# Kernel tuning notes

Measured on AMD Instinct MI355X. Metric: run time of the kernel, lower is better.

Reference implementation:

```python
import jax, jax.numpy as jnp
import numpy as np

WINDOW = 128
CAUSAL = True
LOOK_BACKWARD = 1
LOOK_FORWARD = 0  # causal forces look_forward = 0


def _look_around(x, backward, forward, pad_value, dim):
    # pad along window axis (axis=1), then concat shifted slices along `dim`
    nw = x.shape[1]
    pad_cfg = [(0, 0)] * x.ndim
    pad_cfg[1] = (backward, forward)
    padded = jnp.pad(x, pad_cfg, constant_values=pad_value)
    slices = [padded[:, i:i + nw] for i in range(forward + backward + 1)]
    return jnp.concatenate(slices, axis=dim)


def setup_inputs() -> dict:
    key = jax.random.key(0)
    kq, kk, kv = jax.random.split(key, 3)
    shape = (2, 16, 4096, 64)
    return {
        "q": jax.random.normal(kq, shape, dtype=jnp.float32),
        "k": jax.random.normal(kk, shape, dtype=jnp.float32),
        "v": jax.random.normal(kv, shape, dtype=jnp.float32),
    }


def reference(q, k, v):
    b, h, t, e = q.shape
    scale = e ** (-0.5)
    windows = t // WINDOW  # t assumed divisible by WINDOW (pad_to_multiple is no-op)

    # merge batch and heads, bucket into windows
    bq = q.reshape(b * h, windows, WINDOW, e)
    bk = k.reshape(b * h, windows, WINDOW, e)
    bv = v.reshape(b * h, windows, WINDOW, e)

    # look-around gather of key/value windows: j-dim = WINDOW*(1+back+fwd)
    bk = _look_around(bk, LOOK_BACKWARD, LOOK_FORWARD, 0.0, dim=2)
    bv = _look_around(bv, LOOK_BACKWARD, LOOK_FORWARD, 0.0, dim=2)

    # positional indices for masking
    bq_t = jnp.arange(t).reshape(1, windows, WINDOW)
    bq_k = _look_around(bq_t, LOOK_BACKWARD, LOOK_FORWARD, -1, dim=2)

    mask = (bq_k == -1)[:, :, None, :]  # (1, w, 1, j) padded positions
    if CAUSAL:
        mask = mask | (bq_t[:, :, :, None] < bq_k[:, :, None, :])

    dots = jnp.einsum('bwie,bwje->bwij', bq * scale, bk)
    mask_value = -jnp.finfo(dots.dtype).max
    dots = jnp.where(mask, mask_value, dots)
    attn = jax.nn.softmax(dots.astype(jnp.float32), axis=-1).astype(dots.dtype)
    out = jnp.einsum('bwij,bwje->bwie', attn, bv)
    return out.reshape(b, h, t, e)
```

## Files before the change

kernel.cpp:

```cpp
#include <hip/hip_runtime.h>

#define T_DIM 4096
#define E_DIM 64
#define WIN   128
#define NWIN  (T_DIM / WIN)
#define KS_LD 72
#define VT_ROW 272
#define OS_LD 68

typedef __bf16  bf16x4 __attribute__((ext_vector_type(4)));
typedef __bf16  bf16x8 __attribute__((ext_vector_type(8)));
typedef float   f32x16 __attribute__((ext_vector_type(16)));

__global__ __launch_bounds__(256, 4)
void la_fwd(const float* __restrict__ Q, const float* __restrict__ K,
            const float* __restrict__ V, float* __restrict__ O)
{
  __shared__ __align__(16) unsigned char lds_raw[35840];
  __bf16* Ks  = (__bf16*)(lds_raw);
  char*   Vtb = (char*)(lds_raw + 18432);
  float*  Os  = (float*)(lds_raw);

  const int tid  = threadIdx.x;
  const int lane = tid & 63;
  const int wid  = tid >> 6;
  const int col  = lane & 31;
  const int half = lane >> 5;

  const int flat = blockIdx.x;
  const int w  = (flat >> 3) & 31;
  const int bh = (flat & 7) * 4 + (flat >> 8);

  const float* Qb = Q + (size_t)bh * T_DIM * E_DIM;
  const float* Kb = K + (size_t)bh * T_DIM * E_DIM;
  const float* Vb = V + (size_t)bh * T_DIM * E_DIM;
  float*       Ob = O + (size_t)bh * T_DIM * E_DIM;

  const int q0 = w * WIN;
  const int e0 = (tid & 15) << 2;
  const int jb = (tid >> 4) << 2;

  const float* kp1 = Kb + (size_t)q0 * E_DIM;
  const float* vp1 = Vb + (size_t)q0 * E_DIM;
  const float* kp0 = kp1 - WIN * E_DIM;
  const float* vp0 = vp1 - WIN * E_DIM;

  float4 k0f[8], v0f[8], k1f[8], v1f[8], qf[8];
  if (w > 0) {
#pragma unroll
    for (int i = 0; i < 8; ++i) k0f[i] = *(const float4*)(kp0 + (i << 10) + (tid << 2));
#pragma unroll
    for (int p = 0; p < 2; ++p)
#pragma unroll
      for (int r = 0; r < 4; ++r)
        v0f[p * 4 + r] = *(const float4*)(vp0 + (size_t)(p * 64 + jb + r) * E_DIM + e0);
  }
  {
    const float* qrow = Qb + (size_t)(q0 + wid * 32 + col) * E_DIM;
#pragma unroll
    for (int c = 0; c < 4; ++c) {
      qf[2 * c]     = *(const float4*)(qrow + c * 16 + half * 8);
      qf[2 * c + 1] = *(const float4*)(qrow + c * 16 + half * 8 + 4);
    }
  }
#pragma unroll
  for (int i = 0; i < 8; ++i) k1f[i] = *(const float4*)(kp1 + (i << 10) + (tid << 2));
#pragma unroll
  for (int p = 0; p < 2; ++p)
#pragma unroll
    for (int r = 0; r < 4; ++r)
      v1f[p * 4 + r] = *(const float4*)(vp1 + (size_t)(p * 64 + jb + r) * E_DIM + e0);

  auto cvt8 = [&](const float4* src, bf16x4* dst) {
#pragma unroll
    for (int i = 0; i < 8; ++i) {
      const float* f = (const float*)&src[i];
      bf16x4 b;
      b[0] = (__bf16)f[0]; b[1] = (__bf16)f[1]; b[2] = (__bf16)f[2]; b[3] = (__bf16)f[3];
      dst[i] = b;
    }
  };
  bf16x4 k0b[8], v0b[8], k1b[8], v1b[8];
  if (w > 0) { cvt8(k0f, k0b); cvt8(v0f, v0b); }
  cvt8(k1f, k1b); cvt8(v1f, v1b);

  const float QS = 0.125f * 1.44269504088896340736f;
  bf16x8 bq[4];
#pragma unroll
  for (int c = 0; c < 4; ++c) {
    const float* x = (const float*)&qf[2 * c];
    const float* y = (const float*)&qf[2 * c + 1];
    bf16x8 a;
    a[0]=(__bf16)(x[0]*QS); a[1]=(__bf16)(x[1]*QS); a[2]=(__bf16)(x[2]*QS); a[3]=(__bf16)(x[3]*QS);
    a[4]=(__bf16)(y[0]*QS); a[5]=(__bf16)(y[1]*QS); a[6]=(__bf16)(y[2]*QS); a[7]=(__bf16)(y[3]*QS);
    bq[c] = a;
  }

  auto writeK = [&](const bf16x4* ksrc) {
#pragma unroll
    for (int i = 0; i < 8; ++i) {
      const int fi = (i << 10) + (tid << 2);
      *(bf16x4*)(&Ks[(fi >> 6) * KS_LD + (fi & 63)]) = ksrc[i];
    }
  };
  auto writeV = [&](const bf16x4* vsrc) {
#pragma unroll
    for (int p = 0; p < 2; ++p)
#pragma unroll
      for (int c = 0; c < 4; ++c) {
        bf16x4 t;
        t[0] = vsrc[p*4+0][c]; t[1] = vsrc[p*4+1][c];
        t[2] = vsrc[p*4+2][c]; t[3] = vsrc[p*4+3][c];
        const int e = e0 + c;
        const int boff = (2 * (p * 64 + jb)) ^ (((e >> 3) & 1) << 5);
        *(bf16x4*)(Vtb + e * VT_ROW + boff) = t;
      }
  };

  if (w > 0) { writeK(k0b); writeV(v0b); }
  else       { writeK(k1b); writeV(v1b); }

  float  lsum = 0.0f;
  f32x16 oacc[2];
#pragma unroll
  for (int et = 0; et < 2; ++et)
#pragma unroll
    for (int r = 0; r < 16; ++r) oacc[et][r] = 0.0f;

  __syncthreads();

  auto kb_step = [&](int kb, bool diag) {
    f32x16 s;
#pragma unroll
    for (int r = 0; r < 16; ++r) s[r] = 0.0f;
#pragma unroll
    for (int c = 0; c < 4; ++c) {
      const bf16x8 a = *(const bf16x8*)(&Ks[(kb * 32 + col) * KS_LD + c * 16 + half * 8]);
      s = __builtin_amdgcn_mfma_f32_32x32x16_bf16(a, bq[c], s, 0, 0, 0);
    }
    float pr[16];
#pragma unroll
    for (int r = 0; r < 16; ++r) {
      const int key = (r & 3) + 8 * (r >> 2) + 4 * half;
      float sv = s[r];
      if (diag && key > col) sv = -3.0e38f;
      const float p = __builtin_amdgcn_exp2f(sv);
      lsum += p;
      pr[r] = p;
    }
#pragma unroll
    for (int g = 0; g < 2; ++g) {
      int A0, A1, B0, B1;
      asm("v_cvt_pk_bf16_f32 %0, %1, %2" : "=v"(A0) : "v"(pr[8*g+0]), "v"(pr[8*g+1]));
      asm("v_cvt_pk_bf16_f32 %0, %1, %2" : "=v"(A1) : "v"(pr[8*g+2]), "v"(pr[8*g+3]));
      asm("v_cvt_pk_bf16_f32 %0, %1, %2" : "=v"(B0) : "v"(pr[8*g+4]), "v"(pr[8*g+5]));
      asm("v_cvt_pk_bf16_f32 %0, %1, %2" : "=v"(B1) : "v"(pr[8*g+6]), "v"(pr[8*g+7]));
      asm("v_permlane32_swap_b32 %0, %1" : "+v"(A0), "+v"(B0));
      asm("v_permlane32_swap_b32 %0, %1" : "+v"(A1), "+v"(B1));
      union { int d[4]; bf16x8 v; } u;
      u.d[0] = A0; u.d[1] = A1; u.d[2] = B0; u.d[3] = B1;
      const int j0b = (kb * 64 + g * 32 + half * 16) ^ (((col >> 3) & 1) << 5);
#pragma unroll
      for (int et = 0; et < 2; ++et) {
        const bf16x8 bv = *(const bf16x8*)(Vtb + (et * 32 + col) * VT_ROW + j0b);
        oacc[et] = __builtin_amdgcn_mfma_f32_32x32x16_bf16(u.v, bv, oacc[et], 0, 0, 0);
      }
    }
  };

  if (w > 0) {
#pragma unroll
    for (int kb = 0; kb < 4; ++kb) kb_step(kb, false);
    __syncthreads();
    writeK(k1b); writeV(v1b);
    __syncthreads();
  }
#pragma unroll
  for (int kb = 0; kb < 4; ++kb)
    if (kb <= wid) kb_step(kb, kb == wid);

  float xx = lsum, yy = lsum;
  asm("v_permlane32_swap_b32 %0, %1" : "+v"(xx), "+v"(yy));
  const float ltot = xx + yy;

  __syncthreads();
#pragma unroll
  for (int r = 0; r < 16; ++r) {
    const int row = (r & 3) + 8 * (r >> 2) + 4 * half;
    const float lq   = __int_as_float(__builtin_amdgcn_ds_bpermute(row << 2, __float_as_int(ltot)));
    const float rinv = __builtin_amdgcn_rcpf(lq);
    Os[(wid * 32 + row) * OS_LD + col]      = oacc[0][r] * rinv;
    Os[(wid * 32 + row) * OS_LD + col + 32] = oacc[1][r] * rinv;
  }
  __syncthreads();
  {
    float* ob = Ob + (size_t)q0 * E_DIM;
#pragma unroll
    for (int i = 0; i < 8; ++i) {
      const int fi = (i << 10) + (tid << 2);
      const float4 o4 = *(const float4*)(&Os[(fi >> 6) * OS_LD + (fi & 63)]);
      *(float4*)(ob + fi) = o4;
    }
  }
}

extern "C" void kernel_launch(void* const* d_in, const int* in_sizes, int n_in,
                              void* d_out, int out_size, void* d_ws, size_t ws_size,
                              hipStream_t stream) {
  const float* Q = (const float*)d_in[0];
  const float* K = (const float*)d_in[1];
  const float* V = (const float*)d_in[2];
  float*       O = (float*)d_out;
  const int bh = in_sizes[0] / (T_DIM * E_DIM);
  la_fwd<<<dim3(NWIN * bh), 256, 0, stream>>>(Q, K, V, O);
}
```

Measured before the change: 168.5 us.

## Load second K/V window lazily and simplify transposed V LDS layout

Instead of prefetching both the previous and current K/V windows into registers up front, the kernel now loads, converts and stages each window into LDS only when needed, with the current window fetched after the first window's compute. V is transposed with 8 keys per thread into a padded row stride (136 bf16) instead of an XOR-swizzled layout, writing bf16x8 chunks. This cuts register pressure from holding four windows of float4 data, but puts the second window's global load latency on the critical path between the two compute phases.

New measurement: 140.8 us. 16.4% less time.

```diff
diff --git a/kernel.cpp b/kernel.cpp
--- a/kernel.cpp
+++ b/kernel.cpp
@@ -5,7 +5,7 @@
 #define WIN   128
 #define NWIN  (T_DIM / WIN)
 #define KS_LD 72
-#define VT_ROW 272
+#define VT_LD 136
 #define OS_LD 68
 
 typedef __bf16  bf16x4 __attribute__((ext_vector_type(4)));
@@ -17,9 +17,9 @@
             const float* __restrict__ V, float* __restrict__ O)
 {
   __shared__ __align__(16) unsigned char lds_raw[35840];
-  __bf16* Ks  = (__bf16*)(lds_raw);
-  char*   Vtb = (char*)(lds_raw + 18432);
-  float*  Os  = (float*)(lds_raw);
+  __bf16* Ks = (__bf16*)(lds_raw);
+  __bf16* Vt = (__bf16*)(lds_raw + 18432);
+  float*  Os = (float*)(lds_raw);
 
   const int tid  = threadIdx.x;
   const int lane = tid & 63;
@@ -37,24 +37,42 @@
   float*       Ob = O + (size_t)bh * T_DIM * E_DIM;
 
   const int q0 = w * WIN;
-  const int e0 = (tid & 15) << 2;
-  const int jb = (tid >> 4) << 2;
+  const int eg = tid & 15;
+  const int j0 = (tid >> 4) * 8;
 
   const float* kp1 = Kb + (size_t)q0 * E_DIM;
   const float* vp1 = Vb + (size_t)q0 * E_DIM;
   const float* kp0 = kp1 - WIN * E_DIM;
   const float* vp0 = vp1 - WIN * E_DIM;
 
-  float4 k0f[8], v0f[8], k1f[8], v1f[8], qf[8];
-  if (w > 0) {
+  auto stageK = [&](const float* kp) {
+    float4 kf[8];
 #pragma unroll
-    for (int i = 0; i < 8; ++i) k0f[i] = *(const float4*)(kp0 + (i << 10) + (tid << 2));
+    for (int i = 0; i < 8; ++i) kf[i] = *(const float4*)(kp + (i << 10) + (tid << 2));
 #pragma unroll
-    for (int p = 0; p < 2; ++p)
+    for (int i = 0; i < 8; ++i) {
+      const int fi = (i << 10) + (tid << 2);
+      bf16x4 k4;
+      k4[0]=(__bf16)kf[i].x; k4[1]=(__bf16)kf[i].y; k4[2]=(__bf16)kf[i].z; k4[3]=(__bf16)kf[i].w;
+      *(bf16x4*)(&Ks[(fi >> 6) * KS_LD + (fi & 63)]) = k4;
+    }
+  };
+  auto stageV = [&](const float* vp) {
+    float4 vf[8];
 #pragma unroll
-      for (int r = 0; r < 4; ++r)
-        v0f[p * 4 + r] = *(const float4*)(vp0 + (size_t)(p * 64 + jb + r) * E_DIM + e0);
-  }
+    for (int r = 0; r < 8; ++r)
+      vf[r] = *(const float4*)(vp + (size_t)(j0 + r) * E_DIM + eg * 4);
+#pragma unroll
+    for (int c = 0; c < 4; ++c) {
+      bf16x8 t;
+#pragma unroll
+      for (int r = 0; r < 8; ++r) t[r] = (__bf16)(((const float*)&vf[r])[c]);
+      *(bf16x8*)(&Vt[(eg * 4 + c) * VT_LD + j0]) = t;
+    }
+  };
+
+  const float QS = 0.125f * 1.44269504088896340736f;
+  float4 qf[8];
   {
     const float* qrow = Qb + (size_t)(q0 + wid * 32 + col) * E_DIM;
 #pragma unroll
@@ -63,28 +81,9 @@
       qf[2 * c + 1] = *(const float4*)(qrow + c * 16 + half * 8 + 4);
     }
   }
-#pragma unroll
-  for (int i = 0; i < 8; ++i) k1f[i] = *(const float4*)(kp1 + (i << 10) + (tid << 2));
-#pragma unroll
-  for (int p = 0; p < 2; ++p)
-#pragma unroll
-    for (int r = 0; r < 4; ++r)
-      v1f[p * 4 + r] = *(const float4*)(vp1 + (size_t)(p * 64 + jb + r) * E_DIM + e0);
+  if (w > 0) { stageK(kp0); stageV(vp0); }
+  else       { stageK(kp1); stageV(vp1); }
 
-  auto cvt8 = [&](const float4* src, bf16x4* dst) {
-#pragma unroll
-    for (int i = 0; i < 8; ++i) {
-      const float* f = (const float*)&src[i];
-      bf16x4 b;
-      b[0] = (__bf16)f[0]; b[1] = (__bf16)f[1]; b[2] = (__bf16)f[2]; b[3] = (__bf16)f[3];
-      dst[i] = b;
-    }
-  };
-  bf16x4 k0b[8], v0b[8], k1b[8], v1b[8];
-  if (w > 0) { cvt8(k0f, k0b); cvt8(v0f, v0b); }
-  cvt8(k1f, k1b); cvt8(v1f, v1b);
-
-  const float QS = 0.125f * 1.44269504088896340736f;
   bf16x8 bq[4];
 #pragma unroll
   for (int c = 0; c < 4; ++c) {
@@ -95,30 +94,6 @@
     a[4]=(__bf16)(y[0]*QS); a[5]=(__bf16)(y[1]*QS); a[6]=(__bf16)(y[2]*QS); a[7]=(__bf16)(y[3]*QS);
     bq[c] = a;
   }
-
-  auto writeK = [&](const bf16x4* ksrc) {
-#pragma unroll
-    for (int i = 0; i < 8; ++i) {
-      const int fi = (i << 10) + (tid << 2);
-      *(bf16x4*)(&Ks[(fi >> 6) * KS_LD + (fi & 63)]) = ksrc[i];
-    }
-  };
-  auto writeV = [&](const bf16x4* vsrc) {
-#pragma unroll
-    for (int p = 0; p < 2; ++p)
-#pragma unroll
-      for (int c = 0; c < 4; ++c) {
-        bf16x4 t;
-        t[0] = vsrc[p*4+0][c]; t[1] = vsrc[p*4+1][c];
-        t[2] = vsrc[p*4+2][c]; t[3] = vsrc[p*4+3][c];
-        const int e = e0 + c;
-        const int boff = (2 * (p * 64 + jb)) ^ (((e >> 3) & 1) << 5);
-        *(bf16x4*)(Vtb + e * VT_ROW + boff) = t;
-      }
-  };
-
-  if (w > 0) { writeK(k0b); writeV(v0b); }
-  else       { writeK(k1b); writeV(v1b); }
 
   float  lsum = 0.0f;
   f32x16 oacc[2];
@@ -159,10 +134,10 @@
       asm("v_permlane32_swap_b32 %0, %1" : "+v"(A1), "+v"(B1));
       union { int d[4]; bf16x8 v; } u;
       u.d[0] = A0; u.d[1] = A1; u.d[2] = B0; u.d[3] = B1;
-      const int j0b = (kb * 64 + g * 32 + half * 16) ^ (((col >> 3) & 1) << 5);
+      const int j0v = kb * 32 + g * 16 + half * 8;
 #pragma unroll
       for (int et = 0; et < 2; ++et) {
-        const bf16x8 bv = *(const bf16x8*)(Vtb + (et * 32 + col) * VT_ROW + j0b);
+        const bf16x8 bv = *(const bf16x8*)(&Vt[(et * 32 + col) * VT_LD + j0v]);
         oacc[et] = __builtin_amdgcn_mfma_f32_32x32x16_bf16(u.v, bv, oacc[et], 0, 0, 0);
       }
     }
@@ -172,7 +147,8 @@
 #pragma unroll
     for (int kb = 0; kb < 4; ++kb) kb_step(kb, false);
     __syncthreads();
-    writeK(k1b); writeV(v1b);
+    stageK(kp1);
+    stageV(vp1);
     __syncthreads();
   }
 #pragma unroll
```
